# Optimization experiments

Hardware: AMD Instinct MI355X
Metric: run time of the kernel (lower is better)

Reference implementation:

```python
import jax, jax.numpy as jnp
import numpy as np


def _gru_step(h, x, Wih, Whh, bih, bhh):
    # PyTorch GRU cell: gates ordered (r, z, n)
    gi = x @ Wih.T + bih
    gh = h @ Whh.T + bhh
    ir, iz, inn = jnp.split(gi, 3, axis=-1)
    hr, hz, hn = jnp.split(gh, 3, axis=-1)
    r = jax.nn.sigmoid(ir + hr)
    u = jax.nn.sigmoid(iz + hz)
    n = jnp.tanh(inn + r * hn)
    return (1.0 - u) * n + u * h


def _forward(mini_batch, eps, W_ih1, W_hh1, b_ih1, b_hh1, W_ih2, W_hh2, b_ih2, b_hh2,
             h1_0, h2_0, Wt1, bt1, Wloc, bloc, Wsc, bsc, We1, be1, We2, be2, We3, be3):
    B = mini_batch.shape[0]
    x_tbf = jnp.swapaxes(mini_batch, 0, 1)      # [T,B,dim_x]
    eps_tbf = jnp.swapaxes(eps, 0, 1)           # [T,B,dim_z]
    h2_init = jnp.broadcast_to(h2_0, (B, h2_0.shape[0]))
    h1_init = jnp.broadcast_to(h1_0, (B, h1_0.shape[0]))

    # gen_RNN_2 over full sequence (all seq_lengths == T, pack/pad is identity)
    def scan2(h, x):
        h = _gru_step(h, x, W_ih2, W_hh2, b_ih2, b_hh2)
        return h, h
    _, h2_seq = jax.lax.scan(scan2, h2_init, x_tbf)              # [T,B,dim_h2]
    # at step t the emitter sees h2_output[t-2] (h2_0 for t==1): shift right by one
    h2_shift = jnp.concatenate([h2_init[None], h2_seq[:-1]], axis=0)

    def step(h1, inp):
        eps_t, h2_t = inp
        # stoch_trans (dz): MLP -> z_loc, z_scale
        hid = jax.nn.relu(h1 @ Wt1.T + bt1)
        z_loc = hid @ Wloc.T + bloc
        z_scale = jax.nn.softplus(hid @ Wsc.T + bsc)
        z_t = z_loc + z_scale * eps_t                            # reparameterized sample
        h1n = _gru_step(h1, z_t, W_ih1, W_hh1, b_ih1, b_hh1)     # gen_RNN_1 one step
        dx_in = jnp.concatenate([h1n, h2_t], axis=-1)            # [B, dim_h1+dim_h2]
        e = jax.nn.relu(dx_in @ We1.T + be1)                     # emitter (dx)
        e = jax.nn.relu(e @ We2.T + be2)
        x_ps = jax.nn.sigmoid(e @ We3.T + be3)                   # Bernoulli probs
        return h1n, x_ps

    _, xps = jax.lax.scan(step, h1_init, (eps_tbf, h2_shift))    # [T,B,dim_x]
    return jnp.swapaxes(xps, 0, 1)                               # [B,T,dim_x]


def setup_inputs() -> dict:
    key = jax.random.key(0)
    B, T = 256, 1000
    DX, DZ, H1, H2, DDX, DDZ = 100, 100, 10, 10, 20, 20
    ks = jax.random.split(key, 24)
    f32 = jnp.float32
    w = lambda k, shape: (jax.random.normal(k, shape, f32) * 0.1)
    inp = {
        "mini_batch": (jax.random.uniform(ks[0], (B, T, DX)) < 0.5).astype(f32),
        "eps": jax.random.normal(ks[1], (B, T, DZ), f32),
        # gen_RNN_1: input dim_z -> hidden dim_h1
        "W_ih1": w(ks[2], (3 * H1, DZ)), "W_hh1": w(ks[3], (3 * H1, H1)),
        "b_ih1": w(ks[4], (3 * H1,)), "b_hh1": w(ks[5], (3 * H1,)),
        # gen_RNN_2: input dim_x -> hidden dim_h2
        "W_ih2": w(ks[6], (3 * H2, DX)), "W_hh2": w(ks[7], (3 * H2, H2)),
        "b_ih2": w(ks[8], (3 * H2,)), "b_hh2": w(ks[9], (3 * H2,)),
        "h1_0": jnp.zeros((H1,), f32), "h2_0": jnp.zeros((H2,), f32),
        # stoch_trans (dz): dim_h1 -> dim_dz -> (dim_z loc, dim_z scale)
        "Wt1": w(ks[10], (DDZ, H1)), "bt1": w(ks[11], (DDZ,)),
        "Wloc": w(ks[12], (DZ, DDZ)), "bloc": w(ks[13], (DZ,)),
        "Wsc": w(ks[14], (DZ, DDZ)), "bsc": w(ks[15], (DZ,)),
        # emitter (dx): (dim_h1+dim_h2) -> dim_dx -> dim_dx -> dim_x, sigmoid
        "We1": w(ks[16], (DDX, H1 + H2)), "be1": w(ks[17], (DDX,)),
        "We2": w(ks[18], (DDX, DDX)), "be2": w(ks[19], (DDX,)),
        "We3": w(ks[20], (DX, DDX)), "be3": w(ks[21], (DX,)),
    }
    return inp


def reference(mini_batch, eps, W_ih1, W_hh1, b_ih1, b_hh1, W_ih2, W_hh2, b_ih2, b_hh2,
              h1_0, h2_0, Wt1, bt1, Wloc, bloc, Wsc, bsc, We1, be1, We2, be2, We3, be3):
    return _forward(mini_batch, eps, W_ih1, W_hh1, b_ih1, b_hh1, W_ih2, W_hh2, b_ih2, b_hh2,
                    h1_0, h2_0, Wt1, bt1, Wloc, bloc, Wsc, bsc, We1, be1, We2, be2, We3, be3)
```

## Files before the change

### kernel.cpp

```cpp
#include <hip/hip_runtime.h>
#include <cstdint>

#define T_LEN 1000
#define NB    256

__device__ __forceinline__ float rcpf_(float x)     { return __builtin_amdgcn_rcpf(x); }
__device__ __forceinline__ float sigmoidf_(float x) { return rcpf_(1.f + __expf(-x)); }
__device__ __forceinline__ float tanhf_(float x) {
    float e = __expf(2.f * x);
    return 1.f - 2.f * rcpf_(e + 1.f);
}
__device__ __forceinline__ float softplusf_(float x) {
    return fmaxf(x, 0.f) + __logf(1.f + __expf(-fabsf(x)));
}
__device__ __forceinline__ float bcast_(float v, int l) {
    return __uint_as_float(__builtin_amdgcn_readlane(__float_as_uint(v), l));
}

__global__ __launch_bounds__(256) void gi2_kernel(
    const float* __restrict__ x, const float* __restrict__ W,
    const float* __restrict__ bias, float* __restrict__ out)
{
    __shared__ float xsT[100 * 67];

    const int tid = threadIdx.x;
    const int64_t base = (int64_t)blockIdx.x * (64 * 100);
    const float4* gx = (const float4*)(x + base);

#pragma unroll
    for (int it = 0; it < 7; ++it) {
        int i = tid + it * 256;
        if (i < 1600) {
            int r  = i / 25;
            int k4 = i - r * 25;
            float4 v = gx[i];
            xsT[(4 * k4 + 0) * 67 + r] = v.x;
            xsT[(4 * k4 + 1) * 67 + r] = v.y;
            xsT[(4 * k4 + 2) * 67 + r] = v.z;
            xsT[(4 * k4 + 3) * 67 + r] = v.w;
        }
    }
    __syncthreads();

    const int lane = tid & 63;
    const int wv   = __builtin_amdgcn_readfirstlane(tid >> 6);
    const int j0   = wv * 8;

    float acc[8];
#pragma unroll
    for (int jj = 0; jj < 8; ++jj) acc[jj] = 0.f;

    for (int k = 0; k < 100; ++k) {
        float xv = xsT[k * 67 + lane];
#pragma unroll
        for (int jj = 0; jj < 8; ++jj) {
            int j = j0 + jj; j = j > 29 ? 29 : j;
            acc[jj] = fmaf(xv, W[j * 100 + k], acc[jj]);
        }
    }
    float* orow = out + base + (int64_t)lane * 100;
#pragma unroll
    for (int jj = 0; jj < 8; ++jj) {
        int j = j0 + jj;
        if (j < 30) orow[j] = acc[jj] + bias[j];
    }
}

__global__ __launch_bounds__(128) void scan_kernel(
    const float* __restrict__ eps,
    const float* __restrict__ W_ih1, const float* __restrict__ W_hh1,
    const float* __restrict__ b_ih1, const float* __restrict__ b_hh1,
    const float* __restrict__ W_hh2, const float* __restrict__ b_hh2,
    const float* __restrict__ h1_0,  const float* __restrict__ h2_0,
    const float* __restrict__ Wt1,   const float* __restrict__ bt1,
    const float* __restrict__ Wloc,  const float* __restrict__ bloc,
    const float* __restrict__ Wsc,   const float* __restrict__ bsc,
    const float* __restrict__ We1,   const float* __restrict__ be1,
    const float* __restrict__ We2,   const float* __restrict__ be2,
    const float* __restrict__ We3,   const float* __restrict__ be3,
    float* out)
{
    __shared__ __align__(16) float ss2[2][52];
    __shared__ __align__(16) float sh1ring[2][12];

    const int lane = threadIdx.x & 63;
    const int64_t rowbase = (int64_t)blockIdx.x * T_LEN * 100;
    const int wave = __builtin_amdgcn_readfirstlane((int)(threadIdx.x >> 6));

    if (wave == 0) {
        const int j  = lane & 31;
        const int jc = j < 30 ? j : 29;
        const int h  = lane >> 5;
        const int lt = lane < 20 ? lane : 19;
        const int ls = lane < 50 ? lane : 49;

        float wt1r[10], whh1r[10], wscA[20], wscB[20], wbig[52], Cr[20];
#pragma unroll
        for (int k = 0; k < 10; ++k) {
            wt1r[k]  = Wt1[lt * 10 + k];
            whh1r[k] = W_hh1[jc * 10 + k];
        }
        float bt1r  = bt1[lt];
        float bhh1r = b_hh1[jc];
        float br1   = b_ih1[jc];
#pragma unroll
        for (int l = 0; l < 20; ++l) {
            wscA[l] = Wsc[ls * 20 + l];
            wscB[l] = Wsc[(ls + 50) * 20 + l];
        }
        float bscA = bsc[ls], bscB = bsc[ls + 50];
#pragma unroll
        for (int i = 0; i < 50; ++i) wbig[i] = W_ih1[jc * 100 + h * 50 + i];
        wbig[50] = 0.f; wbig[51] = 0.f;

        float dr = 0.f;
#pragma unroll
        for (int l = 0; l < 20; ++l) Cr[l] = 0.f;
        for (int kk = 0; kk < 100; ++kk) {
            float w = W_ih1[jc * 100 + kk];
            dr = fmaf(w, bloc[kk], dr);
#pragma unroll
            for (int l = 0; l < 20; ++l) Cr[l] = fmaf(w, Wloc[kk * 20 + l], Cr[l]);
        }

        if (lane < 2) { ss2[0][50 + lane] = 0.f; ss2[1][50 + lane] = 0.f; }

        float h1keep = h1_0[lane < 10 ? lane : 0];
        float sh1_[10];
#pragma unroll
        for (int k = 0; k < 10; ++k) sh1_[k] = h1_0[k];

        const float* erow = eps + rowbase;
        float epsA = erow[ls];
        float epsB = erow[ls + 50];

        for (int t = 0; t <= T_LEN; ++t) {
            if (t < T_LEN) {
                float hidv = bt1r, gh1v = bhh1r;
#pragma unroll
                for (int k = 0; k < 10; ++k) {
                    hidv = fmaf(wt1r[k], sh1_[k], hidv);
                    gh1v = fmaf(whh1r[k], sh1_[k], gh1v);
                }
                hidv = fmaxf(hidv, 0.f);

                float sgh[20];
#pragma unroll
                for (int l = 0; l < 20; ++l) sgh[l] = bcast_(hidv, l);

                float scA = bscA, scB = bscB, gq = dr;
#pragma unroll
                for (int l = 0; l < 20; ++l) {
                    scA = fmaf(wscA[l], sgh[l], scA);
                    scB = fmaf(wscB[l], sgh[l], scB);
                    gq  = fmaf(Cr[l],  sgh[l], gq);
                }
                float zA = softplusf_(scA) * epsA;
                float zB = softplusf_(scB) * epsB;
                if (lane < 50) { ss2[0][lane] = zA; ss2[1][lane] = zB; }

                if (t + 1 < T_LEN) {
                    epsA = erow[(t + 1) * 100 + ls];
                    epsB = erow[(t + 1) * 100 + ls + 50];
                }
                __builtin_amdgcn_wave_barrier();

                const float4* sp4 = (const float4*)(&ss2[h][0]);
                float p0 = 0.f, p1 = 0.f, p2 = 0.f, p3 = 0.f;
#pragma unroll
                for (int c = 0; c < 13; ++c) {
                    float4 v = sp4[c];
                    p0 = fmaf(wbig[4 * c + 0], v.x, p0);
                    p1 = fmaf(wbig[4 * c + 1], v.y, p1);
                    p2 = fmaf(wbig[4 * c + 2], v.z, p2);
                    p3 = fmaf(wbig[4 * c + 3], v.w, p3);
                }
                float p = (p0 + p1) + (p2 + p3);
                float gi1v = p + __shfl_xor(p, 32) + br1 + gq;
                float av   = gi1v + gh1v;
                float a10  = __shfl(av,   lane + 10);
                float gin  = __shfl(gi1v, lane + 20);
                float ghn  = __shfl(gh1v, lane + 20);
                if (lane < 10) {
                    float r = sigmoidf_(av);
                    float u = sigmoidf_(a10);
                    float n = tanhf_(fmaf(r, ghn, gin));
                    h1keep = fmaf(u, h1keep - n, n);
                    sh1ring[t & 1][lane] = h1keep;
                }
#pragma unroll
                for (int k = 0; k < 10; ++k) sh1_[k] = bcast_(h1keep, k);
            }
            __syncthreads();
        }
    } else {
        const int lt20 = lane < 20 ? lane : 19;
        const int l30  = lane < 30 ? lane : 29;
        const int ls   = lane < 50 ? lane : 49;

        float whh2r[10];
#pragma unroll
        for (int k = 0; k < 10; ++k) whh2r[k] = W_hh2[l30 * 10 + k];
        float bhh2r = b_hh2[l30];

        float we1r[20], we2r[20], we3A[20], we3B[20];
#pragma unroll
        for (int k = 0; k < 20; ++k) {
            we1r[k] = We1[lt20 * 20 + k];
            we2r[k] = We2[lt20 * 20 + k];
            we3A[k] = We3[ls * 20 + k];
            we3B[k] = We3[(ls + 50) * 20 + k];
        }
        float be1r = be1[lt20], be2r = be2[lt20];
        float be3A = be3[ls],   be3B = be3[ls + 50];

        float h2keep = h2_0[lane < 10 ? lane : 0];
        float g2c[10], g2p[10];
#pragma unroll
        for (int k = 0; k < 10; ++k) { g2c[k] = h2_0[k]; g2p[k] = h2_0[k]; }

        float gi2reg = out[rowbase + l30];

        for (int t = 0; t <= T_LEN; ++t) {
            float4 d0 = make_float4(0.f, 0.f, 0.f, 0.f);
            float4 d1 = d0; float d8 = 0.f, d9 = 0.f;
            if (t >= 1) {
                const int s1 = (t - 1) & 1;
                d0 = *(const float4*)(&sh1ring[s1][0]);
                d1 = *(const float4*)(&sh1ring[s1][4]);
                d8 = sh1ring[s1][8]; d9 = sh1ring[s1][9];
            }

            const bool upd = (t < T_LEN);
            if (upd) {
                float gh2v = bhh2r;
#pragma unroll
                for (int k = 0; k < 10; ++k) gh2v = fmaf(whh2r[k], g2c[k], gh2v);
                float gi2v = gi2reg;
                if (t + 1 < T_LEN)
                    gi2reg = out[rowbase + (int64_t)(t + 1) * 100 + l30];
                float a2  = gi2v + gh2v;
                float a10 = __shfl(a2,   lane + 10);
                float gin = __shfl(gi2v, lane + 20);
                float ghn = __shfl(gh2v, lane + 20);
                if (lane < 10) {
                    float r = sigmoidf_(a2);
                    float u = sigmoidf_(a10);
                    float n = tanhf_(fmaf(r, ghn, gin));
                    h2keep = fmaf(u, h2keep - n, n);
                }
            }

            if (t >= 1) {
                float e1v = be1r;
                e1v = fmaf(we1r[0], d0.x, e1v); e1v = fmaf(we1r[1], d0.y, e1v);
                e1v = fmaf(we1r[2], d0.z, e1v); e1v = fmaf(we1r[3], d0.w, e1v);
                e1v = fmaf(we1r[4], d1.x, e1v); e1v = fmaf(we1r[5], d1.y, e1v);
                e1v = fmaf(we1r[6], d1.z, e1v); e1v = fmaf(we1r[7], d1.w, e1v);
                e1v = fmaf(we1r[8], d8,   e1v); e1v = fmaf(we1r[9], d9,   e1v);
#pragma unroll
                for (int k = 0; k < 10; ++k) e1v = fmaf(we1r[10 + k], g2p[k], e1v);
                e1v = fmaxf(e1v, 0.f);

                float se1v[20];
#pragma unroll
                for (int l = 0; l < 20; ++l) se1v[l] = bcast_(e1v, l);

                float e2v = be2r;
#pragma unroll
                for (int k = 0; k < 20; ++k) e2v = fmaf(we2r[k], se1v[k], e2v);
                e2v = fmaxf(e2v, 0.f);

                float se2v[20];
#pragma unroll
                for (int l = 0; l < 20; ++l) se2v[l] = bcast_(e2v, l);

                float xA = be3A, xB = be3B;
#pragma unroll
                for (int l = 0; l < 20; ++l) {
                    xA = fmaf(we3A[l], se2v[l], xA);
                    xB = fmaf(we3B[l], se2v[l], xB);
                }
                xA = sigmoidf_(xA);
                xB = sigmoidf_(xB);
                if (lane < 50) {
                    int64_t ro = rowbase + (int64_t)(t - 1) * 100;
                    out[ro + lane]      = xA;
                    out[ro + lane + 50] = xB;
                }
            }

            if (upd) {
#pragma unroll
                for (int k = 0; k < 10; ++k) g2p[k] = g2c[k];
#pragma unroll
                for (int k = 0; k < 10; ++k) g2c[k] = bcast_(h2keep, k);
            }
            __syncthreads();
        }
    }
}

extern "C" void kernel_launch(void* const* d_in, const int* in_sizes, int n_in,
                              void* d_out, int out_size, void* d_ws, size_t ws_size,
                              hipStream_t stream) {
    const float* mini_batch = (const float*)d_in[0];
    const float* eps        = (const float*)d_in[1];
    const float* W_ih1      = (const float*)d_in[2];
    const float* W_hh1      = (const float*)d_in[3];
    const float* b_ih1      = (const float*)d_in[4];
    const float* b_hh1      = (const float*)d_in[5];
    const float* W_ih2      = (const float*)d_in[6];
    const float* W_hh2      = (const float*)d_in[7];
    const float* b_ih2      = (const float*)d_in[8];
    const float* b_hh2      = (const float*)d_in[9];
    const float* h1_0       = (const float*)d_in[10];
    const float* h2_0       = (const float*)d_in[11];
    const float* Wt1        = (const float*)d_in[12];
    const float* bt1        = (const float*)d_in[13];
    const float* Wloc       = (const float*)d_in[14];
    const float* bloc       = (const float*)d_in[15];
    const float* Wsc        = (const float*)d_in[16];
    const float* bsc        = (const float*)d_in[17];
    const float* We1        = (const float*)d_in[18];
    const float* be1        = (const float*)d_in[19];
    const float* We2        = (const float*)d_in[20];
    const float* be2        = (const float*)d_in[21];
    const float* We3        = (const float*)d_in[22];
    const float* be3        = (const float*)d_in[23];
    float* out = (float*)d_out;

    gi2_kernel<<<(NB * T_LEN) / 64, 256, 0, stream>>>(mini_batch, W_ih2, b_ih2, out);

    scan_kernel<<<NB, 128, 0, stream>>>(eps, W_ih1, W_hh1, b_ih1, b_hh1, W_hh2, b_hh2,
                                        h1_0, h2_0, Wt1, bt1, Wloc, bloc, Wsc, bsc,
                                        We1, be1, We2, be2, We3, be3, out);
}
```

Measured before the change: 751.6 us.

## Merge scan's two waves into one wave with manual 2-step unroll

Collapses the two-wave scan kernel (one wave for the h1/z recurrence, one for the h2 GRU and emitter) into a single 64-thread wave per batch row. This removes the per-step __syncthreads and the shared h1 ring buffer. The h2 GRU and the emitter for step t-1 are interleaved with the h1 dependency chain so their work can fill latency on the serial path. The loop is unrolled by two with ping-pong register buffers and prefetches eps and gi2 two steps ahead, and dot products are split into two accumulators to shorten FMA chains. The cost is that one wave now does all the arithmetic serially and holds far more live registers.

```diff
diff --git a/kernel.cpp b/kernel.cpp
--- a/kernel.cpp
+++ b/kernel.cpp
@@ -66,7 +66,140 @@
     }
 }
 
-__global__ __launch_bounds__(128) void scan_kernel(
+
+#define EMIT_STEP(S, G2Pn)                                               \
+    do {                                                                 \
+        float ea_ = be1r, eb_ = 0.f;                                     \
+        _Pragma("unroll")                                                \
+        for (int k_ = 0; k_ < 5; ++k_) {                                 \
+            ea_ = fmaf(we1r[2*k_],        sh1_[2*k_],     ea_);          \
+            eb_ = fmaf(we1r[2*k_+1],      sh1_[2*k_+1],   eb_);          \
+            ea_ = fmaf(we1r[10+2*k_],     (G2Pn)[2*k_],   ea_);          \
+            eb_ = fmaf(we1r[10+2*k_+1],   (G2Pn)[2*k_+1], eb_);          \
+        }                                                                \
+        float e1v_ = fmaxf(ea_ + eb_, 0.f);                              \
+        float se1_[20];                                                  \
+        _Pragma("unroll")                                                \
+        for (int l_ = 0; l_ < 20; ++l_) se1_[l_] = bcast_(e1v_, l_);     \
+        float fa_ = be2r, fb_ = 0.f;                                     \
+        _Pragma("unroll")                                                \
+        for (int k_ = 0; k_ < 10; ++k_) {                                \
+            fa_ = fmaf(we2r[2*k_],   se1_[2*k_],   fa_);                 \
+            fb_ = fmaf(we2r[2*k_+1], se1_[2*k_+1], fb_);                 \
+        }                                                                \
+        float e2v_ = fmaxf(fa_ + fb_, 0.f);                              \
+        float se2_[20];                                                  \
+        _Pragma("unroll")                                                \
+        for (int l_ = 0; l_ < 20; ++l_) se2_[l_] = bcast_(e2v_, l_);     \
+        float xa0_ = be3A, xa1_ = 0.f, xb0_ = be3B, xb1_ = 0.f;          \
+        _Pragma("unroll")                                                \
+        for (int l_ = 0; l_ < 10; ++l_) {                                \
+            xa0_ = fmaf(we3A[2*l_],   se2_[2*l_],   xa0_);               \
+            xa1_ = fmaf(we3A[2*l_+1], se2_[2*l_+1], xa1_);               \
+            xb0_ = fmaf(we3B[2*l_],   se2_[2*l_],   xb0_);               \
+            xb1_ = fmaf(we3B[2*l_+1], se2_[2*l_+1], xb1_);               \
+        }                                                                \
+        float xA_ = sigmoidf_(xa0_ + xa1_);                              \
+        float xB_ = sigmoidf_(xb0_ + xb1_);                              \
+        if (lane < 50) {                                                 \
+            int64_t ro_ = rowbase + (int64_t)(S) * 100;                  \
+            out[ro_ + lane]      = xA_;                                  \
+            out[ro_ + lane + 50] = xB_;                                  \
+        }                                                                \
+    } while (0)
+
+#define STEP_BODY(T, EA, EB, GC, G2C, G2P)                               \
+    do {                                                                 \
+        float ha_ = bt1r, hb_ = 0.f, ga_ = bhh1r, gb_ = 0.f;             \
+        _Pragma("unroll")                                                \
+        for (int k_ = 0; k_ < 5; ++k_) {                                 \
+            ha_ = fmaf(wt1r[2*k_],    sh1_[2*k_],   ha_);                \
+            hb_ = fmaf(wt1r[2*k_+1],  sh1_[2*k_+1], hb_);                \
+            ga_ = fmaf(whh1r[2*k_],   sh1_[2*k_],   ga_);                \
+            gb_ = fmaf(whh1r[2*k_+1], sh1_[2*k_+1], gb_);                \
+        }                                                                \
+        float hidv_ = fmaxf(ha_ + hb_, 0.f);                             \
+        float gh1v_ = ga_ + gb_;                                         \
+        float sgh_[20];                                                  \
+        _Pragma("unroll")                                                \
+        for (int l_ = 0; l_ < 20; ++l_) sgh_[l_] = bcast_(hidv_, l_);    \
+        float sA0_ = bscx, sA1_ = 0.f, sB0_ = bscy, sB1_ = 0.f;          \
+        float q0_ = dr, q1_ = 0.f;                                       \
+        _Pragma("unroll")                                                \
+        for (int l_ = 0; l_ < 10; ++l_) {                                \
+            sA0_ = fmaf(wscA[2*l_],   sgh_[2*l_],   sA0_);               \
+            sA1_ = fmaf(wscA[2*l_+1], sgh_[2*l_+1], sA1_);               \
+            sB0_ = fmaf(wscB[2*l_],   sgh_[2*l_],   sB0_);               \
+            sB1_ = fmaf(wscB[2*l_+1], sgh_[2*l_+1], sB1_);               \
+            q0_  = fmaf(Cr[2*l_],     sgh_[2*l_],   q0_);                \
+            q1_  = fmaf(Cr[2*l_+1],   sgh_[2*l_+1], q1_);                \
+        }                                                                \
+        float gq_ = q0_ + q1_;                                           \
+        float zA_ = softplusf_(sA0_ + sA1_) * (EA);                      \
+        float zB_ = softplusf_(sB0_ + sB1_) * (EB);                      \
+        if (lane < 50) { ss[lane] = zA_; ss[52 + lane] = zB_; }          \
+        {                                                                \
+            int tp_ = (T) + 2 < T_LEN ? (T) + 2 : T_LEN - 1;             \
+            const float* ep_ = erow + (int64_t)tp_ * 100;                \
+            (EA) = ep_[ls];                                              \
+            (EB) = ep_[ls + 50];                                         \
+        }                                                                \
+        float g2a_ = bhh2r, g2b_ = 0.f;                                  \
+        _Pragma("unroll")                                                \
+        for (int k_ = 0; k_ < 5; ++k_) {                                 \
+            g2a_ = fmaf(whh2r[2*k_],   (G2C)[2*k_],   g2a_);             \
+            g2b_ = fmaf(whh2r[2*k_+1], (G2C)[2*k_+1], g2b_);             \
+        }                                                                \
+        float gh2v_ = g2a_ + g2b_;                                       \
+        float gi2v_ = (GC);                                              \
+        {                                                                \
+            int tp_ = (T) + 2 < T_LEN ? (T) + 2 : T_LEN - 1;             \
+            (GC) = out[rowbase + (int64_t)tp_ * 100 + l30];              \
+        }                                                                \
+        float a2_   = gi2v_ + gh2v_;                                     \
+        float a210_ = __shfl(a2_,   lane + 10);                          \
+        float g2in_ = __shfl(gi2v_, lane + 20);                          \
+        float g2hn_ = __shfl(gh2v_, lane + 20);                          \
+        if (lane < 10) {                                                 \
+            float r_ = sigmoidf_(a2_);                                   \
+            float u_ = sigmoidf_(a210_);                                 \
+            float n_ = tanhf_(fmaf(r_, g2hn_, g2in_));                   \
+            h2keep = fmaf(u_, h2keep - n_, n_);                          \
+        }                                                                \
+        if ((T) >= 1) EMIT_STEP((T) - 1, G2P);                           \
+        __builtin_amdgcn_wave_barrier();                                 \
+        {                                                                \
+            const float4* sp4_ = (const float4*)(&ss[52 * h]);           \
+            float p0_ = 0.f, p1_ = 0.f, p2_ = 0.f, p3_ = 0.f;            \
+            _Pragma("unroll")                                            \
+            for (int c_ = 0; c_ < 13; ++c_) {                            \
+                float4 v_ = sp4_[c_];                                    \
+                p0_ = fmaf(wbig[4*c_+0], v_.x, p0_);                     \
+                p1_ = fmaf(wbig[4*c_+1], v_.y, p1_);                     \
+                p2_ = fmaf(wbig[4*c_+2], v_.z, p2_);                     \
+                p3_ = fmaf(wbig[4*c_+3], v_.w, p3_);                     \
+            }                                                            \
+            float p_ = (p0_ + p1_) + (p2_ + p3_);                        \
+            float gi1v_ = p_ + __shfl_xor(p_, 32) + br1 + gq_;           \
+            float av_   = gi1v_ + gh1v_;                                 \
+            float a110_ = __shfl(av_,   lane + 10);                      \
+            float g1in_ = __shfl(gi1v_, lane + 20);                      \
+            float g1hn_ = __shfl(gh1v_, lane + 20);                      \
+            if (lane < 10) {                                             \
+                float r_ = sigmoidf_(av_);                               \
+                float u_ = sigmoidf_(a110_);                             \
+                float n_ = tanhf_(fmaf(r_, g1hn_, g1in_));               \
+                h1keep = fmaf(u_, h1keep - n_, n_);                      \
+            }                                                            \
+        }                                                                \
+        _Pragma("unroll")                                                \
+        for (int k_ = 0; k_ < 10; ++k_) {                                \
+            sh1_[k_]  = bcast_(h1keep, k_);                              \
+            (G2P)[k_] = bcast_(h2keep, k_);                              \
+        }                                                                \
+    } while (0)
+
+__global__ __launch_bounds__(64) void scan_kernel(
     const float* __restrict__ eps,
     const float* __restrict__ W_ih1, const float* __restrict__ W_hh1,
     const float* __restrict__ b_ih1, const float* __restrict__ b_hh1,
@@ -80,225 +213,79 @@
     const float* __restrict__ We3,   const float* __restrict__ be3,
     float* out)
 {
-    __shared__ __align__(16) float ss2[2][52];
-    __shared__ __align__(16) float sh1ring[2][12];
-
-    const int lane = threadIdx.x & 63;
-    const int64_t rowbase = (int64_t)blockIdx.x * T_LEN * 100;
-    const int wave = __builtin_amdgcn_readfirstlane((int)(threadIdx.x >> 6));
-
-    if (wave == 0) {
-        const int j  = lane & 31;
-        const int jc = j < 30 ? j : 29;
-        const int h  = lane >> 5;
-        const int lt = lane < 20 ? lane : 19;
-        const int ls = lane < 50 ? lane : 49;
-
-        float wt1r[10], whh1r[10], wscA[20], wscB[20], wbig[52], Cr[20];
-#pragma unroll
-        for (int k = 0; k < 10; ++k) {
-            wt1r[k]  = Wt1[lt * 10 + k];
-            whh1r[k] = W_hh1[jc * 10 + k];
-        }
-        float bt1r  = bt1[lt];
-        float bhh1r = b_hh1[jc];
-        float br1   = b_ih1[jc];
-#pragma unroll
-        for (int l = 0; l < 20; ++l) {
-            wscA[l] = Wsc[ls * 20 + l];
-            wscB[l] = Wsc[(ls + 50) * 20 + l];
-        }
-        float bscA = bsc[ls], bscB = bsc[ls + 50];
-#pragma unroll
-        for (int i = 0; i < 50; ++i) wbig[i] = W_ih1[jc * 100 + h * 50 + i];
-        wbig[50] = 0.f; wbig[51] = 0.f;
-
-        float dr = 0.f;
-#pragma unroll
-        for (int l = 0; l < 20; ++l) Cr[l] = 0.f;
-        for (int kk = 0; kk < 100; ++kk) {
-            float w = W_ih1[jc * 100 + kk];
-            dr = fmaf(w, bloc[kk], dr);
-#pragma unroll
-            for (int l = 0; l < 20; ++l) Cr[l] = fmaf(w, Wloc[kk * 20 + l], Cr[l]);
-        }
-
-        if (lane < 2) { ss2[0][50 + lane] = 0.f; ss2[1][50 + lane] = 0.f; }
-
-        float h1keep = h1_0[lane < 10 ? lane : 0];
-        float sh1_[10];
-#pragma unroll
-        for (int k = 0; k < 10; ++k) sh1_[k] = h1_0[k];
-
-        const float* erow = eps + rowbase;
-        float epsA = erow[ls];
-        float epsB = erow[ls + 50];
-
-        for (int t = 0; t <= T_LEN; ++t) {
-            if (t < T_LEN) {
-                float hidv = bt1r, gh1v = bhh1r;
-#pragma unroll
-                for (int k = 0; k < 10; ++k) {
-                    hidv = fmaf(wt1r[k], sh1_[k], hidv);
-                    gh1v = fmaf(whh1r[k], sh1_[k], gh1v);
-                }
-                hidv = fmaxf(hidv, 0.f);
-
-                float sgh[20];
-#pragma unroll
-                for (int l = 0; l < 20; ++l) sgh[l] = bcast_(hidv, l);
-
-                float scA = bscA, scB = bscB, gq = dr;
-#pragma unroll
-                for (int l = 0; l < 20; ++l) {
-                    scA = fmaf(wscA[l], sgh[l], scA);
-                    scB = fmaf(wscB[l], sgh[l], scB);
-                    gq  = fmaf(Cr[l],  sgh[l], gq);
-                }
-                float zA = softplusf_(scA) * epsA;
-                float zB = softplusf_(scB) * epsB;
-                if (lane < 50) { ss2[0][lane] = zA; ss2[1][lane] = zB; }
-
-                if (t + 1 < T_LEN) {
-                    epsA = erow[(t + 1) * 100 + ls];
-                    epsB = erow[(t + 1) * 100 + ls + 50];
-                }
-                __builtin_amdgcn_wave_barrier();
-
-                const float4* sp4 = (const float4*)(&ss2[h][0]);
-                float p0 = 0.f, p1 = 0.f, p2 = 0.f, p3 = 0.f;
-#pragma unroll
-                for (int c = 0; c < 13; ++c) {
-                    float4 v = sp4[c];
-                    p0 = fmaf(wbig[4 * c + 0], v.x, p0);
-                    p1 = fmaf(wbig[4 * c + 1], v.y, p1);
-                    p2 = fmaf(wbig[4 * c + 2], v.z, p2);
-                    p3 = fmaf(wbig[4 * c + 3], v.w, p3);
-                }
-                float p = (p0 + p1) + (p2 + p3);
-                float gi1v = p + __shfl_xor(p, 32) + br1 + gq;
-                float av   = gi1v + gh1v;
-                float a10  = __shfl(av,   lane + 10);
-                float gin  = __shfl(gi1v, lane + 20);
-                float ghn  = __shfl(gh1v, lane + 20);
-                if (lane < 10) {
-                    float r = sigmoidf_(av);
-                    float u = sigmoidf_(a10);
-                    float n = tanhf_(fmaf(r, ghn, gin));
-                    h1keep = fmaf(u, h1keep - n, n);
-                    sh1ring[t & 1][lane] = h1keep;
-                }
-#pragma unroll
-                for (int k = 0; k < 10; ++k) sh1_[k] = bcast_(h1keep, k);
-            }
-            __syncthreads();
-        }
-    } else {
-        const int lt20 = lane < 20 ? lane : 19;
-        const int l30  = lane < 30 ? lane : 29;
-        const int ls   = lane < 50 ? lane : 49;
-
-        float whh2r[10];
-#pragma unroll
-        for (int k = 0; k < 10; ++k) whh2r[k] = W_hh2[l30 * 10 + k];
-        float bhh2r = b_hh2[l30];
-
-        float we1r[20], we2r[20], we3A[20], we3B[20];
-#pragma unroll
-        for (int k = 0; k < 20; ++k) {
-            we1r[k] = We1[lt20 * 20 + k];
-            we2r[k] = We2[lt20 * 20 + k];
-            we3A[k] = We3[ls * 20 + k];
-            we3B[k] = We3[(ls + 50) * 20 + k];
-        }
-        float be1r = be1[lt20], be2r = be2[lt20];
-        float be3A = be3[ls],   be3B = be3[ls + 50];
-
-        float h2keep = h2_0[lane < 10 ? lane : 0];
-        float g2c[10], g2p[10];
-#pragma unroll
-        for (int k = 0; k < 10; ++k) { g2c[k] = h2_0[k]; g2p[k] = h2_0[k]; }
-
-        float gi2reg = out[rowbase + l30];
-
-        for (int t = 0; t <= T_LEN; ++t) {
-            float4 d0 = make_float4(0.f, 0.f, 0.f, 0.f);
-            float4 d1 = d0; float d8 = 0.f, d9 = 0.f;
-            if (t >= 1) {
-                const int s1 = (t - 1) & 1;
-                d0 = *(const float4*)(&sh1ring[s1][0]);
-                d1 = *(const float4*)(&sh1ring[s1][4]);
-                d8 = sh1ring[s1][8]; d9 = sh1ring[s1][9];
-            }
-
-            const bool upd = (t < T_LEN);
-            if (upd) {
-                float gh2v = bhh2r;
-#pragma unroll
-                for (int k = 0; k < 10; ++k) gh2v = fmaf(whh2r[k], g2c[k], gh2v);
-                float gi2v = gi2reg;
-                if (t + 1 < T_LEN)
-                    gi2reg = out[rowbase + (int64_t)(t + 1) * 100 + l30];
-                float a2  = gi2v + gh2v;
-                float a10 = __shfl(a2,   lane + 10);
-                float gin = __shfl(gi2v, lane + 20);
-                float ghn = __shfl(gh2v, lane + 20);
-                if (lane < 10) {
-                    float r = sigmoidf_(a2);
-                    float u = sigmoidf_(a10);
-                    float n = tanhf_(fmaf(r, ghn, gin));
-                    h2keep = fmaf(u, h2keep - n, n);
-                }
-            }
-
-            if (t >= 1) {
-                float e1v = be1r;
-                e1v = fmaf(we1r[0], d0.x, e1v); e1v = fmaf(we1r[1], d0.y, e1v);
-                e1v = fmaf(we1r[2], d0.z, e1v); e1v = fmaf(we1r[3], d0.w, e1v);
-                e1v = fmaf(we1r[4], d1.x, e1v); e1v = fmaf(we1r[5], d1.y, e1v);
-                e1v = fmaf(we1r[6], d1.z, e1v); e1v = fmaf(we1r[7], d1.w, e1v);
-                e1v = fmaf(we1r[8], d8,   e1v); e1v = fmaf(we1r[9], d9,   e1v);
-#pragma unroll
-                for (int k = 0; k < 10; ++k) e1v = fmaf(we1r[10 + k], g2p[k], e1v);
-                e1v = fmaxf(e1v, 0.f);
-
-                float se1v[20];
-#pragma unroll
-                for (int l = 0; l < 20; ++l) se1v[l] = bcast_(e1v, l);
-
-                float e2v = be2r;
-#pragma unroll
-                for (int k = 0; k < 20; ++k) e2v = fmaf(we2r[k], se1v[k], e2v);
-                e2v = fmaxf(e2v, 0.f);
-
-                float se2v[20];
-#pragma unroll
-                for (int l = 0; l < 20; ++l) se2v[l] = bcast_(e2v, l);
-
-                float xA = be3A, xB = be3B;
-#pragma unroll
-                for (int l = 0; l < 20; ++l) {
-                    xA = fmaf(we3A[l], se2v[l], xA);
-                    xB = fmaf(we3B[l], se2v[l], xB);
-                }
-                xA = sigmoidf_(xA);
-                xB = sigmoidf_(xB);
-                if (lane < 50) {
-                    int64_t ro = rowbase + (int64_t)(t - 1) * 100;
-                    out[ro + lane]      = xA;
-                    out[ro + lane + 50] = xB;
-                }
-            }
-
-            if (upd) {
-#pragma unroll
-                for (int k = 0; k < 10; ++k) g2p[k] = g2c[k];
-#pragma unroll
-                for (int k = 0; k < 10; ++k) g2c[k] = bcast_(h2keep, k);
-            }
-            __syncthreads();
-        }
-    }
+    __shared__ __align__(16) float ss[104];
+
+    const int lane = threadIdx.x;
+    const int64_t rowbase = (int64_t)blockIdx.x * (T_LEN * 100);
+
+    const int j   = lane & 31;
+    const int jc  = j < 30 ? j : 29;
+    const int h   = lane >> 5;
+    const int lt  = lane < 20 ? lane : 19;
+    const int ls  = lane < 50 ? lane : 49;
+    const int l30 = lane < 30 ? lane : 29;
+
+    float wt1r[10], whh1r[10], whh2r[10];
+    float wscA[20], wscB[20], Cr[20], we1r[20], we2r[20], we3A[20], we3B[20];
+    float wbig[52];
+
+#pragma unroll
+    for (int k = 0; k < 10; ++k) {
+        wt1r[k]  = Wt1[lt * 10 + k];
+        whh1r[k] = W_hh1[jc * 10 + k];
+        whh2r[k] = W_hh2[l30 * 10 + k];
+    }
+    float bt1r = bt1[lt], bhh1r = b_hh1[jc], br1 = b_ih1[jc], bhh2r = b_hh2[l30];
+#pragma unroll
+    for (int l = 0; l < 20; ++l) {
+        wscA[l] = Wsc[ls * 20 + l];
+        wscB[l] = Wsc[(ls + 50) * 20 + l];
+        we1r[l] = We1[lt * 20 + l];
+        we2r[l] = We2[lt * 20 + l];
+        we3A[l] = We3[ls * 20 + l];
+        we3B[l] = We3[(ls + 50) * 20 + l];
+    }
+    float bscx = bsc[ls], bscy = bsc[ls + 50];
+    float be1r = be1[lt], be2r = be2[lt];
+    float be3A = be3[ls], be3B = be3[ls + 50];
+#pragma unroll
+    for (int i = 0; i < 50; ++i) wbig[i] = W_ih1[jc * 100 + h * 50 + i];
+    wbig[50] = 0.f; wbig[51] = 0.f;
+
+    float dr = 0.f;
+#pragma unroll
+    for (int l = 0; l < 20; ++l) Cr[l] = 0.f;
+    for (int kk = 0; kk < 100; ++kk) {
+        float w = W_ih1[jc * 100 + kk];
+        dr = fmaf(w, bloc[kk], dr);
+#pragma unroll
+        for (int l = 0; l < 20; ++l) Cr[l] = fmaf(w, Wloc[kk * 20 + l], Cr[l]);
+    }
+
+    if (lane < 2) { ss[50 + lane] = 0.f; ss[102 + lane] = 0.f; }
+
+    float h1keep = h1_0[lane < 10 ? lane : 0];
+    float h2keep = h2_0[lane < 10 ? lane : 0];
+    float sh1_[10], g2U[10], g2V[10];
+#pragma unroll
+    for (int k = 0; k < 10; ++k) {
+        sh1_[k] = h1_0[k];
+        g2U[k]  = h2_0[k];
+        g2V[k]  = h2_0[k];
+    }
+
+    const float* erow = eps + rowbase;
+    float eA0 = erow[ls],       eB0 = erow[ls + 50];
+    float eA1 = erow[100 + ls], eB1 = erow[100 + ls + 50];
+    float gC0 = out[rowbase + l30];
+    float gC1 = out[rowbase + 100 + l30];
+
+#pragma unroll 1
+    for (int tt = 0; tt < T_LEN; tt += 2) {
+        STEP_BODY(tt,     eA0, eB0, gC0, g2U, g2V);
+        STEP_BODY(tt + 1, eA1, eB1, gC1, g2V, g2U);
+    }
+    EMIT_STEP(T_LEN - 1, g2V);
 }
 
 extern "C" void kernel_launch(void* const* d_in, const int* in_sizes, int n_in,
@@ -332,7 +319,7 @@
 
     gi2_kernel<<<(NB * T_LEN) / 64, 256, 0, stream>>>(mini_batch, W_ih2, b_ih2, out);
 
-    scan_kernel<<<NB, 128, 0, stream>>>(eps, W_ih1, W_hh1, b_ih1, b_hh1, W_hh2, b_hh2,
-                                        h1_0, h2_0, Wt1, bt1, Wloc, bloc, Wsc, bsc,
-                                        We1, be1, We2, be2, We3, be3, out);
-}
+    scan_kernel<<<NB, 64, 0, stream>>>(eps, W_ih1, W_hh1, b_ih1, b_hh1, W_hh2, b_hh2,
+                                       h1_0, h2_0, Wt1, bt1, Wloc, bloc, Wsc, bsc,
+                                       We1, be1, We2, be2, We3, be3, out);
+}
```

Measured after the change: 1.322 ms. 75.9% more time.
